# Kernel optimization log

Measured on AMD Instinct MI355X. Metric: run time of the kernel, lower is better.

## Reference

```python
import jax, jax.numpy as jnp
import numpy as np

B, IN, HID, OUT = 1024, 512, 128, 64
INP1 = IN + 1  # 513, after prepending ones column


def setup_inputs() -> dict:
    key = jax.random.key(0)
    k1, k2, k3, k4, k5, k6, k7, k8 = jax.random.split(key, 8)
    s1 = 1.0 / np.sqrt(INP1 * INP1)
    s2 = 1.0 / np.sqrt(HID)
    return {
        "img": jax.random.normal(k1, (B, IN), dtype=jnp.float32),
        "tab": jax.random.normal(k2, (B, IN), dtype=jnp.float32),
        "W1": jax.random.uniform(k3, (HID, INP1 * INP1), jnp.float32, -s1, s1),
        "b1": jax.random.uniform(k4, (HID,), jnp.float32, -s1, s1),
        "W2": jax.random.uniform(k5, (HID, HID), jnp.float32, -s2, s2),
        "b2": jax.random.uniform(k6, (HID,), jnp.float32, -s2, s2),
        "W3": jax.random.uniform(k7, (OUT, HID), jnp.float32, -s2, s2),
        "b3": jax.random.uniform(k8, (OUT,), jnp.float32, -s2, s2),
    }


def reference(img, tab, W1, b1, W2, b2, W3, b3):
    ones = jnp.ones((img.shape[0], 1), dtype=img.dtype)
    x = jnp.concatenate([ones, img], axis=1)  # [B, IN+1]
    t = jnp.concatenate([ones, tab], axis=1)  # [B, IN+1]
    # batched outer product, flattened: [B, (IN+1)*(IN+1)]
    fusion = jnp.einsum("bi,bj->bij", x, t).reshape(x.shape[0], -1)
    # dropout is identity in eval mode
    y1 = fusion @ W1.T + b1
    y2 = jnp.tanh(y1 @ W2.T + b2)
    y3 = jax.nn.relu(y2 @ W3.T + b3)
    return y3
```

## Files before the change

### kernel.cpp

```cpp
#include <hip/hip_runtime.h>
#include <hip/hip_bf16.h>

typedef __bf16 bf16x8 __attribute__((ext_vector_type(8)));
typedef float f32x4 __attribute__((ext_vector_type(4)));
typedef float f32x4u __attribute__((ext_vector_type(4), aligned(4)));
typedef unsigned short u16x8 __attribute__((ext_vector_type(8)));

typedef __attribute__((address_space(1))) const unsigned int gu32;
typedef __attribute__((address_space(3))) unsigned int lu32;

#define B_SZ   1024
#define IN_SZ  512
#define HID    128
#define OUT_SZ 64
#define BK     32
#define NKT    16

static __device__ __forceinline__ unsigned short f2bf(float f) {
    __hip_bfloat16 h = __float2bfloat16(f);
    return *reinterpret_cast<unsigned short*>(&h);
}

__global__ __launch_bounds__(256) void prep_kernel(
    const float* __restrict__ img, const float* __restrict__ tab,
    unsigned short* __restrict__ tbt, float* __restrict__ xhT,
    float* __restrict__ tc)
{
    const int blk = blockIdx.x;
    for (int j = threadIdx.x; j < 512; j += 256) {
        float v = (j == 0) ? 1.0f : tab[(size_t)blk * IN_SZ + (j - 1)];
        tbt[(size_t)blk * 512 + j] = f2bf(v);
    }
    if (threadIdx.x == 0) tc[blk] = tab[(size_t)blk * IN_SZ + 511];
    if (blk < 513) {
        for (int b = threadIdx.x; b < B_SZ; b += 256)
            xhT[(size_t)blk * B_SZ + b] =
                (blk == 0) ? 1.0f : img[(size_t)b * IN_SZ + (blk - 1)];
    }
}

__global__ __launch_bounds__(256) void prep2_kernel(
    const float* __restrict__ w1, unsigned short* __restrict__ w1b)
{
    const long long gid = (long long)blockIdx.x * 256 + threadIdx.x;
    const int r  = (int)(gid >> 6);
    const int c8 = ((int)gid & 63) << 3;
    const float* src = w1 + (size_t)r * 513 + c8;
    const f32x4u lo = *reinterpret_cast<const f32x4u*>(src);
    const f32x4u hi = *reinterpret_cast<const f32x4u*>(src + 4);
    u16x8 u;
    u[0] = f2bf(lo[0]); u[1] = f2bf(lo[1]); u[2] = f2bf(lo[2]); u[3] = f2bf(lo[3]);
    u[4] = f2bf(hi[0]); u[5] = f2bf(hi[1]); u[6] = f2bf(hi[2]); u[7] = f2bf(hi[3]);
    *reinterpret_cast<u16x8*>(w1b + (size_t)r * 512 + c8) = u;
}

__global__ __launch_bounds__(512, 4) void gemm_fused(
    const float* __restrict__ w1, const unsigned short* __restrict__ w1b,
    const unsigned short* __restrict__ tbt,
    const float* __restrict__ xhT, const float* __restrict__ tc,
    float* __restrict__ y1acc)
{
    __shared__ unsigned short Als[3][128 * BK];
    __shared__ unsigned short Bls[3][256 * BK];

    int wgid;
    {
        const int orig = blockIdx.x;
        const int xcd = orig & 7;
        const int pos = orig >> 3;
        wgid = (xcd < 4 ? xcd * 257 : 4 * 257 + (xcd - 4) * 256) + pos;
    }
    const int bm = wgid >> 2;
    const int bn = wgid & 3;
    const int m0 = bm * 128;
    const int n0 = bn * 256;
    const int tid  = threadIdx.x;
    const int wv   = tid >> 6;
    const int wr   = wv >> 2;
    const int wc   = wv & 3;
    const int lane = tid & 63;
    const int l15  = lane & 15;
    const int kg   = lane >> 4;

    const unsigned short* asrc;
    {
        const int r  = tid >> 2;
        const int cl = (tid & 3) ^ ((r >> 1) & 3);
        asrc = w1b + (size_t)(m0 + r) * 512 + cl * 8;
    }
    const int aBase = (wv * 64) * 8;

    const unsigned short* bsrc[2];
    int bBase[2];
    #pragma unroll
    for (int q = 0; q < 2; ++q) {
        const int p  = q * 512 + tid;
        const int r  = p >> 2;
        const int cl = (p & 3) ^ ((r >> 1) & 3);
        bsrc[q] = tbt + (size_t)(n0 + r) * 512 + cl * 8;
        bBase[q] = (q * 512 + wv * 64) * 8;
    }

    int aoffs[4], boffs[4];
    #pragma unroll
    for (int ms = 0; ms < 4; ++ms) {
        const int r = wr * 64 + ms * 16 + l15;
        aoffs[ms] = (r * 4 + (kg ^ ((r >> 1) & 3))) * 8;
    }
    #pragma unroll
    for (int ns = 0; ns < 4; ++ns) {
        const int r = wc * 64 + ns * 16 + l15;
        boffs[ns] = (r * 4 + (kg ^ ((r >> 1) & 3))) * 8;
    }

    f32x4 acc[4][4] = {};

#define STAGE(BUF, KT) do {                                                  \
        const int k32_ = (KT) * BK;                                          \
        __builtin_amdgcn_global_load_lds(                                    \
            (gu32*)(const void*)(asrc + k32_),                               \
            (lu32*)(void*)&Als[BUF][aBase], 16, 0, 0);                       \
        _Pragma("unroll")                                                    \
        for (int q_ = 0; q_ < 2; ++q_)                                       \
            __builtin_amdgcn_global_load_lds(                                \
                (gu32*)(const void*)(bsrc[q_] + k32_),                       \
                (lu32*)(void*)&Bls[BUF][bBase[q_]], 16, 0, 0);               \
    } while (0)

    STAGE(0, 0);
    STAGE(1, 1);

    #pragma unroll
    for (int kt = 0; kt < NKT; ++kt) {
        if (kt == NKT - 1) asm volatile("s_waitcnt vmcnt(0)" ::: "memory");
        else               asm volatile("s_waitcnt vmcnt(3)" ::: "memory");
        __builtin_amdgcn_s_barrier();
        __builtin_amdgcn_sched_barrier(0);

        if (kt + 2 < NKT) STAGE((kt + 2) % 3, kt + 2);

        const int cur = kt % 3;
        const unsigned short* ab = &Als[cur][0];
        const unsigned short* bb = &Bls[cur][0];
        bf16x8 af[4], bfr[4];
        #pragma unroll
        for (int ms = 0; ms < 4; ++ms)
            af[ms] = *reinterpret_cast<const bf16x8*>(&ab[aoffs[ms]]);
        #pragma unroll
        for (int ns = 0; ns < 4; ++ns)
            bfr[ns] = *reinterpret_cast<const bf16x8*>(&bb[boffs[ns]]);
        __builtin_amdgcn_s_setprio(1);
        #pragma unroll
        for (int ms = 0; ms < 4; ++ms)
            #pragma unroll
            for (int ns = 0; ns < 4; ++ns)
                acc[ms][ns] = __builtin_amdgcn_mfma_f32_16x16x32_bf16(
                    af[ms], bfr[ns], acc[ms][ns], 0, 0, 0);
        __builtin_amdgcn_s_setprio(0);
    }
#undef STAGE

    const int h0 = m0 / 513;
    const int mb = (h0 + 1) * 513;
    const bool cross = (mb < m0 + 128);

    float wcv[4][4];
    #pragma unroll
    for (int ms = 0; ms < 4; ++ms)
        #pragma unroll
        for (int v = 0; v < 4; ++v)
            wcv[ms][v] = w1[(size_t)(m0 + wr * 64 + ms * 16 + kg * 4 + v) * 513 + 512];

    #pragma unroll
    for (int ns = 0; ns < 4; ++ns) {
        const int ncol = n0 + wc * 64 + ns * 16 + l15;
        const float tv = tc[ncol];
        float s0 = 0.f, s1 = 0.f;
        #pragma unroll
        for (int ms = 0; ms < 4; ++ms) {
            #pragma unroll
            for (int v = 0; v < 4; ++v) {
                const int m = m0 + wr * 64 + ms * 16 + kg * 4 + v;
                const bool lo = (m < mb);
                const int i = lo ? (m - h0 * 513) : (m - mb);
                const float xv = xhT[(size_t)i * B_SZ + ncol];
                const float val = (acc[ms][ns][v] + wcv[ms][v] * tv) * xv;
                if (lo) s0 += val; else s1 += val;
            }
        }
        s0 += __shfl_xor(s0, 16); s0 += __shfl_xor(s0, 32);
        if (lane < 16) atomicAdd(&y1acc[(size_t)ncol * HID + h0], s0);
        if (cross) {
            s1 += __shfl_xor(s1, 16); s1 += __shfl_xor(s1, 32);
            if (lane < 16 && (h0 + 1) < HID)
                atomicAdd(&y1acc[(size_t)ncol * HID + h0 + 1], s1);
        }
    }
}

__global__ __launch_bounds__(512, 4) void gemm_fused_fb(
    const float* __restrict__ w1, const unsigned short* __restrict__ tbt,
    const float* __restrict__ xhT, const float* __restrict__ tc,
    float* __restrict__ y1acc)
{
    __shared__ float          Afs[2][64 * BK];
    __shared__ unsigned short Bls[2][512 * BK];

    const int bm = blockIdx.x >> 1;
    const int bn = blockIdx.x & 1;
    const int m0 = bm * 64;
    const int n0 = bn * 512;
    const int tid  = threadIdx.x;
    const int wv   = tid >> 6;
    const int lane = tid & 63;
    const int l15  = lane & 15;
    const int kg   = lane >> 4;

    const int ar  = tid >> 3;
    const int acl = (tid & 7) ^ (ar & 7);
    const float* asrc = w1 + (size_t)(m0 + ar) * 513 + acl * 4;
    const int aBase = (wv * 64) * 4;

    const unsigned short* bsrc[4];
    int bBase[4];
    #pragma unroll
    for (int q = 0; q < 4; ++q) {
        const int p  = q * 512 + tid;
        const int r  = p >> 2;
        const int cl = (p & 3) ^ ((r >> 1) & 3);
        bsrc[q] = tbt + (size_t)(n0 + r) * 512 + cl * 8;
        bBase[q] = (q * 512 + wv * 64) * 8;
    }

    int aoff0[4], aoff1[4], boffs[4];
    #pragma unroll
    for (int ms = 0; ms < 4; ++ms) {
        const int r = ms * 16 + l15;
        aoff0[ms] = r * 32 + (((kg * 2) + 0) ^ (r & 7)) * 4;
        aoff1[ms] = r * 32 + (((kg * 2) + 1) ^ (r & 7)) * 4;
    }
    #pragma unroll
    for (int ns = 0; ns < 4; ++ns) {
        const int r = wv * 64 + ns * 16 + l15;
        boffs[ns] = ((r << 2) | (kg ^ ((r >> 1) & 3))) * 8;
    }

    f32x4 acc[4][4] = {};

#define STAGE_FB(BUF, KT) do {                                               \
        const int k32_ = (KT) * BK;                                          \
        _Pragma("unroll")                                                    \
        for (int q_ = 0; q_ < 4; ++q_)                                       \
            __builtin_amdgcn_global_load_lds(                                \
                (gu32*)(const void*)(bsrc[q_] + k32_),                       \
                (lu32*)(void*)&Bls[BUF][bBase[q_]], 16, 0, 0);               \
        __builtin_amdgcn_global_load_lds(                                    \
            (gu32*)(const void*)(asrc + k32_),                               \
            (lu32*)(void*)&Afs[BUF][aBase], 16, 0, 0);                       \
    } while (0)

    STAGE_FB(0, 0);
    __syncthreads();

    for (int kt = 0; kt < NKT; ++kt) {
        const int cur = kt & 1;
        if (kt + 1 < NKT) STAGE_FB(cur ^ 1, kt + 1);

        const float*          ab = &Afs[cur][0];
        const unsigned short* bb = &Bls[cur][0];
        bf16x8 bfr[4];
        #pragma unroll
        for (int ns = 0; ns < 4; ++ns)
            bfr[ns] = *reinterpret_cast<const bf16x8*>(&bb[boffs[ns]]);
        #pragma unroll
        for (int ms = 0; ms < 4; ++ms) {
            const f32x4 lo = *reinterpret_cast<const f32x4*>(&ab[aoff0[ms]]);
            const f32x4 hi = *reinterpret_cast<const f32x4*>(&ab[aoff1[ms]]);
            u16x8 u;
            u[0] = f2bf(lo[0]); u[1] = f2bf(lo[1]);
            u[2] = f2bf(lo[2]); u[3] = f2bf(lo[3]);
            u[4] = f2bf(hi[0]); u[5] = f2bf(hi[1]);
            u[6] = f2bf(hi[2]); u[7] = f2bf(hi[3]);
            const bf16x8 af = __builtin_bit_cast(bf16x8, u);
            #pragma unroll
            for (int ns = 0; ns < 4; ++ns)
                acc[ms][ns] = __builtin_amdgcn_mfma_f32_16x16x32_bf16(
                    af, bfr[ns], acc[ms][ns], 0, 0, 0);
        }
        __syncthreads();
    }
#undef STAGE_FB

    const int h0 = m0 / 513;
    const int mb = (h0 + 1) * 513;
    const bool cross = (mb < m0 + 64);

    float wcv[4][4];
    #pragma unroll
    for (int ms = 0; ms < 4; ++ms)
        #pragma unroll
        for (int v = 0; v < 4; ++v)
            wcv[ms][v] = w1[(size_t)(m0 + ms * 16 + kg * 4 + v) * 513 + 512];

    #pragma unroll
    for (int ns = 0; ns < 4; ++ns) {
        const int ncol = n0 + wv * 64 + ns * 16 + l15;
        const float tv = tc[ncol];
        float s0 = 0.f, s1 = 0.f;
        #pragma unroll
        for (int ms = 0; ms < 4; ++ms) {
            #pragma unroll
            for (int v = 0; v < 4; ++v) {
                const int m = m0 + ms * 16 + kg * 4 + v;
                const bool lo = (m < mb);
                const int i = lo ? (m - h0 * 513) : (m - mb);
                const float xv = xhT[(size_t)i * B_SZ + ncol];
                const float val = (acc[ms][ns][v] + wcv[ms][v] * tv) * xv;
                if (lo) s0 += val; else s1 += val;
            }
        }
        s0 += __shfl_xor(s0, 16); s0 += __shfl_xor(s0, 32);
        if (lane < 16) atomicAdd(&y1acc[(size_t)ncol * HID + h0], s0);
        if (cross) {
            s1 += __shfl_xor(s1, 16); s1 += __shfl_xor(s1, 32);
            if (lane < 16 && (h0 + 1) < HID)
                atomicAdd(&y1acc[(size_t)ncol * HID + h0 + 1], s1);
        }
    }
}

__global__ __launch_bounds__(128) void mlp_kernel(
    const float* __restrict__ y1acc, const float* __restrict__ b1,
    const float* __restrict__ W2, const float* __restrict__ b2,
    const float* __restrict__ W3, const float* __restrict__ b3,
    float* __restrict__ out)
{
    __shared__ float y1r[HID];
    __shared__ float y2r[HID];
    const int b = blockIdx.x;
    const int h = threadIdx.x;
    y1r[h] = y1acc[(size_t)b * HID + h] + b1[h];
    __syncthreads();
    float a = b2[h];
    const float* w2r = W2 + (size_t)h * HID;
    #pragma unroll 8
    for (int k = 0; k < HID; ++k) a += w2r[k] * y1r[k];
    y2r[h] = tanhf(a);
    __syncthreads();
    if (h < OUT_SZ) {
        float a3 = b3[h];
        const float* w3r = W3 + (size_t)h * HID;
        #pragma unroll 8
        for (int k = 0; k < HID; ++k) a3 += w3r[k] * y2r[k];
        out[(size_t)b * OUT_SZ + h] = fmaxf(a3, 0.f);
    }
}

extern "C" void kernel_launch(void* const* d_in, const int* in_sizes, int n_in,
                              void* d_out, int out_size, void* d_ws, size_t ws_size,
                              hipStream_t stream) {
    const float* img = (const float*)d_in[0];
    const float* tab = (const float*)d_in[1];
    const float* W1  = (const float*)d_in[2];
    const float* b1  = (const float*)d_in[3];
    const float* W2  = (const float*)d_in[4];
    const float* b2  = (const float*)d_in[5];
    const float* W3  = (const float*)d_in[6];
    const float* b3  = (const float*)d_in[7];
    float* out = (float*)d_out;

    char* ws = (char*)d_ws;
    float*          y1acc = (float*)ws;
    unsigned short* tbt   = (unsigned short*)(ws + 524288);
    float*          xhT   = (float*)(ws + 1572864);
    float*          tc    = (float*)(ws + 3674112);
    unsigned short* w1b   = (unsigned short*)(ws + 3678208);
    const size_t need = 3678208ULL + 67239936ULL;

    hipMemsetAsync(y1acc, 0, (size_t)B_SZ * HID * sizeof(float), stream);
    prep_kernel<<<dim3(1024), dim3(256), 0, stream>>>(img, tab, tbt, xhT, tc);
    if (ws_size >= need) {
        prep2_kernel<<<dim3(65664 * 64 / 256), dim3(256), 0, stream>>>(W1, w1b);
        gemm_fused<<<dim3(2052), dim3(512), 0, stream>>>(W1, w1b, tbt, xhT, tc, y1acc);
    } else {
        gemm_fused_fb<<<dim3(2052), dim3(512), 0, stream>>>(W1, tbt, xhT, tc, y1acc);
    }
    mlp_kernel<<<dim3(1024), dim3(128), 0, stream>>>(y1acc, b1, W2, b2, W3, b3, out);
}
```

Before: 188.3 us.

## Enlarge W1 GEMM tile to 256x256 with BK=64 quarter-phased pipeline

The main bf16 GEMM tile grows from 128x256 to 256x256, so each workgroup holds 8x4 accumulator fragments and loads tiles with BK=64 into two double-buffered halves. A new 32-phase loop interleaves quarter-tile LDS fragment reads and global-to-LDS prefetches with MFMA blocks, aiming to raise arithmetic intensity and overlap loads with compute. W1 rows are padded to a multiple of 256 with zeros in the conversion kernel, and the grid is halved. The larger tile increases register and LDS use and cuts occupancy to 2 waves per SIMD, and it adds more barriers per k-step.

```diff
diff --git a/kernel.cpp b/kernel.cpp
--- a/kernel.cpp
+++ b/kernel.cpp
@@ -15,6 +15,8 @@
 #define OUT_SZ 64
 #define BK     32
 #define NKT    16
+#define M_REAL 65664
+#define M_PAD  65792
 
 static __device__ __forceinline__ unsigned short f2bf(float f) {
     __hip_bfloat16 h = __float2bfloat16(f);
@@ -45,34 +47,38 @@
     const long long gid = (long long)blockIdx.x * 256 + threadIdx.x;
     const int r  = (int)(gid >> 6);
     const int c8 = ((int)gid & 63) << 3;
-    const float* src = w1 + (size_t)r * 513 + c8;
-    const f32x4u lo = *reinterpret_cast<const f32x4u*>(src);
-    const f32x4u hi = *reinterpret_cast<const f32x4u*>(src + 4);
     u16x8 u;
-    u[0] = f2bf(lo[0]); u[1] = f2bf(lo[1]); u[2] = f2bf(lo[2]); u[3] = f2bf(lo[3]);
-    u[4] = f2bf(hi[0]); u[5] = f2bf(hi[1]); u[6] = f2bf(hi[2]); u[7] = f2bf(hi[3]);
+    if (r < M_REAL) {
+        const float* src = w1 + (size_t)r * 513 + c8;
+        const f32x4u lo = *reinterpret_cast<const f32x4u*>(src);
+        const f32x4u hi = *reinterpret_cast<const f32x4u*>(src + 4);
+        u[0] = f2bf(lo[0]); u[1] = f2bf(lo[1]); u[2] = f2bf(lo[2]); u[3] = f2bf(lo[3]);
+        u[4] = f2bf(hi[0]); u[5] = f2bf(hi[1]); u[6] = f2bf(hi[2]); u[7] = f2bf(hi[3]);
+    } else {
+        u = (u16x8){0,0,0,0,0,0,0,0};
+    }
     *reinterpret_cast<u16x8*>(w1b + (size_t)r * 512 + c8) = u;
 }
 
-__global__ __launch_bounds__(512, 4) void gemm_fused(
+__global__ __launch_bounds__(512, 2) void gemm_fused(
     const float* __restrict__ w1, const unsigned short* __restrict__ w1b,
     const unsigned short* __restrict__ tbt,
     const float* __restrict__ xhT, const float* __restrict__ tc,
     float* __restrict__ y1acc)
 {
-    __shared__ unsigned short Als[3][128 * BK];
-    __shared__ unsigned short Bls[3][256 * BK];
+    __shared__ unsigned short Als[2 * 2 * 8192];
+    __shared__ unsigned short Bls[2 * 2 * 8192];
 
     int wgid;
     {
         const int orig = blockIdx.x;
         const int xcd = orig & 7;
         const int pos = orig >> 3;
-        wgid = (xcd < 4 ? xcd * 257 : 4 * 257 + (xcd - 4) * 256) + pos;
+        wgid = (xcd < 4 ? xcd * 129 : 4 * 129 + (xcd - 4) * 128) + pos;
     }
     const int bm = wgid >> 2;
     const int bn = wgid & 3;
-    const int m0 = bm * 128;
+    const int m0 = bm * 256;
     const int n0 = bn * 256;
     const int tid  = threadIdx.x;
     const int wv   = tid >> 6;
@@ -82,109 +88,153 @@
     const int l15  = lane & 15;
     const int kg   = lane >> 4;
 
-    const unsigned short* asrc;
-    {
-        const int r  = tid >> 2;
-        const int cl = (tid & 3) ^ ((r >> 1) & 3);
-        asrc = w1b + (size_t)(m0 + r) * 512 + cl * 8;
-    }
-    const int aBase = (wv * 64) * 8;
-
-    const unsigned short* bsrc[2];
-    int bBase[2];
-    #pragma unroll
-    for (int q = 0; q < 2; ++q) {
-        const int p  = q * 512 + tid;
-        const int r  = p >> 2;
-        const int cl = (p & 3) ^ ((r >> 1) & 3);
-        bsrc[q] = tbt + (size_t)(n0 + r) * 512 + cl * 8;
-        bBase[q] = (q * 512 + wv * 64) * 8;
-    }
-
-    int aoffs[4], boffs[4];
-    #pragma unroll
-    for (int ms = 0; ms < 4; ++ms) {
-        const int r = wr * 64 + ms * 16 + l15;
-        aoffs[ms] = (r * 4 + (kg ^ ((r >> 1) & 3))) * 8;
-    }
-    #pragma unroll
-    for (int ns = 0; ns < 4; ++ns) {
-        const int r = wc * 64 + ns * 16 + l15;
-        boffs[ns] = (r * 4 + (kg ^ ((r >> 1) & 3))) * 8;
-    }
-
-    f32x4 acc[4][4] = {};
-
-#define STAGE(BUF, KT) do {                                                  \
-        const int k32_ = (KT) * BK;                                          \
-        __builtin_amdgcn_global_load_lds(                                    \
-            (gu32*)(const void*)(asrc + k32_),                               \
-            (lu32*)(void*)&Als[BUF][aBase], 16, 0, 0);                       \
-        _Pragma("unroll")                                                    \
-        for (int q_ = 0; q_ < 2; ++q_)                                       \
-            __builtin_amdgcn_global_load_lds(                                \
-                (gu32*)(const void*)(bsrc[q_] + k32_),                       \
-                (lu32*)(void*)&Bls[BUF][bBase[q_]], 16, 0, 0);               \
+    const unsigned short* aS[2][2];
+    int aD[2];
+    const unsigned short* bS[2][2];
+    int bD[2];
+    #pragma unroll
+    for (int cq = 0; cq < 2; ++cq) {
+        const int p  = cq * 512 + tid;
+        const int rr = p >> 3;
+        const int lc = (p & 7) ^ (rr & 7);
+        {
+            const int wr_ = rr >> 6, j = rr & 63;
+            aS[cq][0] = w1b + (size_t)(m0 + wr_ * 128 +      j) * 512 + lc * 8;
+            aS[cq][1] = w1b + (size_t)(m0 + wr_ * 128 + 64 + j) * 512 + lc * 8;
+        }
+        {
+            const int wc_ = rr >> 5, j2 = rr & 31;
+            bS[cq][0] = tbt + (size_t)(n0 + wc_ * 64 +      j2) * 512 + lc * 8;
+            bS[cq][1] = tbt + (size_t)(n0 + wc_ * 64 + 32 + j2) * 512 + lc * 8;
+        }
+        aD[cq] = p * 8;
+        bD[cq] = p * 8;
+    }
+
+    int aoff[4][2], boff[2][2];
+    #pragma unroll
+    for (int mf = 0; mf < 4; ++mf)
+        #pragma unroll
+        for (int ks = 0; ks < 2; ++ks) {
+            const int rr = wr * 64 + mf * 16 + l15;
+            aoff[mf][ks] = rr * 64 + ((ks * 4 + kg) ^ (rr & 7)) * 8;
+        }
+    #pragma unroll
+    for (int fr = 0; fr < 2; ++fr)
+        #pragma unroll
+        for (int ks = 0; ks < 2; ++ks) {
+            const int rr = wc * 32 + fr * 16 + l15;
+            boff[fr][ks] = rr * 64 + ((ks * 4 + kg) ^ (rr & 7)) * 8;
+        }
+
+    f32x4 acc[8][4] = {};
+    bf16x8 fA[4][2], fB[2][2][2];
+
+#define GL(SRC, DST) __builtin_amdgcn_global_load_lds(                       \
+        (gu32*)(const void*)(SRC), (lu32*)(void*)(DST), 16, 0, 0)
+#define STA(T, H) do {                                                       \
+        unsigned short* b_ = &Als[((((T) & 1) << 1) + (H)) * 8192];          \
+        GL(aS[0][H] + (T) * 64, b_ + aD[0]);                                 \
+        GL(aS[1][H] + (T) * 64, b_ + aD[1]);                                 \
     } while (0)
-
-    STAGE(0, 0);
-    STAGE(1, 1);
-
-    #pragma unroll
-    for (int kt = 0; kt < NKT; ++kt) {
-        if (kt == NKT - 1) asm volatile("s_waitcnt vmcnt(0)" ::: "memory");
-        else               asm volatile("s_waitcnt vmcnt(3)" ::: "memory");
+#define STB(T, H) do {                                                       \
+        unsigned short* b_ = &Bls[((((T) & 1) << 1) + (H)) * 8192];          \
+        GL(bS[0][H] + (T) * 64, b_ + bD[0]);                                 \
+        GL(bS[1][H] + (T) * 64, b_ + bD[1]);                                 \
+    } while (0)
+
+    STA(0, 0); STB(0, 0); STA(0, 1); STB(0, 1); STA(1, 0); STB(1, 0);
+    asm volatile("s_waitcnt vmcnt(4)" ::: "memory");
+    __builtin_amdgcn_s_barrier();
+
+    #pragma unroll
+    for (int P = 0; P < 32; ++P) {
+        const int kt = P >> 2, q = P & 3, d = kt & 1, mh = q >> 1, nq = q & 1;
+        const unsigned short* Ab = &Als[((d << 1) + mh) * 8192];
+        const unsigned short* Bb = &Bls[((d << 1) + nq) * 8192];
+
+        if (q == 0) {
+            #pragma unroll
+            for (int mf = 0; mf < 4; ++mf)
+                #pragma unroll
+                for (int ks = 0; ks < 2; ++ks)
+                    fA[mf][ks] = *reinterpret_cast<const bf16x8*>(&Ab[aoff[mf][ks]]);
+            #pragma unroll
+            for (int fr = 0; fr < 2; ++fr)
+                #pragma unroll
+                for (int ks = 0; ks < 2; ++ks)
+                    fB[0][fr][ks] = *reinterpret_cast<const bf16x8*>(&Bb[boff[fr][ks]]);
+            if (kt + 1 <= 7) STA(kt + 1, 1);
+        } else if (q == 1) {
+            #pragma unroll
+            for (int fr = 0; fr < 2; ++fr)
+                #pragma unroll
+                for (int ks = 0; ks < 2; ++ks)
+                    fB[1][fr][ks] = *reinterpret_cast<const bf16x8*>(&Bb[boff[fr][ks]]);
+            if (kt + 1 <= 7) STB(kt + 1, 1);
+        } else if (q == 2) {
+            #pragma unroll
+            for (int mf = 0; mf < 4; ++mf)
+                #pragma unroll
+                for (int ks = 0; ks < 2; ++ks)
+                    fA[mf][ks] = *reinterpret_cast<const bf16x8*>(&Ab[aoff[mf][ks]]);
+            if (kt + 2 <= 7) STA(kt + 2, 0);
+        } else {
+            if (kt + 2 <= 7) STB(kt + 2, 0);
+        }
+
         __builtin_amdgcn_s_barrier();
+        asm volatile("s_waitcnt lgkmcnt(0)" ::: "memory");
         __builtin_amdgcn_sched_barrier(0);
-
-        if (kt + 2 < NKT) STAGE((kt + 2) % 3, kt + 2);
-
-        const int cur = kt % 3;
-        const unsigned short* ab = &Als[cur][0];
-        const unsigned short* bb = &Bls[cur][0];
-        bf16x8 af[4], bfr[4];
-        #pragma unroll
-        for (int ms = 0; ms < 4; ++ms)
-            af[ms] = *reinterpret_cast<const bf16x8*>(&ab[aoffs[ms]]);
-        #pragma unroll
-        for (int ns = 0; ns < 4; ++ns)
-            bfr[ns] = *reinterpret_cast<const bf16x8*>(&bb[boffs[ns]]);
         __builtin_amdgcn_s_setprio(1);
         #pragma unroll
-        for (int ms = 0; ms < 4; ++ms)
-            #pragma unroll
-            for (int ns = 0; ns < 4; ++ns)
-                acc[ms][ns] = __builtin_amdgcn_mfma_f32_16x16x32_bf16(
-                    af[ms], bfr[ns], acc[ms][ns], 0, 0, 0);
+        for (int mf = 0; mf < 4; ++mf)
+            #pragma unroll
+            for (int fr = 0; fr < 2; ++fr)
+                #pragma unroll
+                for (int ks = 0; ks < 2; ++ks)
+                    acc[mh * 4 + mf][nq * 2 + fr] =
+                        __builtin_amdgcn_mfma_f32_16x16x32_bf16(
+                            fA[mf][ks], fB[nq][fr][ks],
+                            acc[mh * 4 + mf][nq * 2 + fr], 0, 0, 0);
         __builtin_amdgcn_s_setprio(0);
-    }
-#undef STAGE
+        if (q == 3) {
+            if (kt >= 6) asm volatile("s_waitcnt vmcnt(0)" ::: "memory");
+            else         asm volatile("s_waitcnt vmcnt(4)" ::: "memory");
+        }
+        __builtin_amdgcn_s_barrier();
+    }
+#undef STA
+#undef STB
+#undef GL
 
     const int h0 = m0 / 513;
     const int mb = (h0 + 1) * 513;
-    const bool cross = (mb < m0 + 128);
-
-    float wcv[4][4];
-    #pragma unroll
-    for (int ms = 0; ms < 4; ++ms)
-        #pragma unroll
-        for (int v = 0; v < 4; ++v)
-            wcv[ms][v] = w1[(size_t)(m0 + wr * 64 + ms * 16 + kg * 4 + v) * 513 + 512];
-
-    #pragma unroll
-    for (int ns = 0; ns < 4; ++ns) {
-        const int ncol = n0 + wc * 64 + ns * 16 + l15;
+    const bool cross = (mb < m0 + 256);
+
+    float wcv[8][4];
+    #pragma unroll
+    for (int am = 0; am < 8; ++am)
+        #pragma unroll
+        for (int v = 0; v < 4; ++v) {
+            const int g = m0 + wr * 128 + am * 16 + kg * 4 + v;
+            wcv[am][v] = (g < M_REAL) ? w1[(size_t)g * 513 + 512] : 0.f;
+        }
+
+    #pragma unroll
+    for (int an = 0; an < 4; ++an) {
+        const int ncol = n0 + wc * 64 + an * 16 + l15;
         const float tv = tc[ncol];
         float s0 = 0.f, s1 = 0.f;
         #pragma unroll
-        for (int ms = 0; ms < 4; ++ms) {
+        for (int am = 0; am < 8; ++am) {
             #pragma unroll
             for (int v = 0; v < 4; ++v) {
-                const int m = m0 + wr * 64 + ms * 16 + kg * 4 + v;
+                const int m = m0 + wr * 128 + am * 16 + kg * 4 + v;
                 const bool lo = (m < mb);
                 const int i = lo ? (m - h0 * 513) : (m - mb);
-                const float xv = xhT[(size_t)i * B_SZ + ncol];
-                const float val = (acc[ms][ns][v] + wcv[ms][v] * tv) * xv;
+                const float val = (acc[am][an][v] + wcv[am][v] * tv)
+                                  * xhT[(size_t)i * B_SZ + ncol];
                 if (lo) s0 += val; else s1 += val;
             }
         }
@@ -314,8 +364,8 @@
                 const int m = m0 + ms * 16 + kg * 4 + v;
                 const bool lo = (m < mb);
                 const int i = lo ? (m - h0 * 513) : (m - mb);
-                const float xv = xhT[(size_t)i * B_SZ + ncol];
-                const float val = (acc[ms][ns][v] + wcv[ms][v] * tv) * xv;
+                const float val = (acc[ms][ns][v] + wcv[ms][v] * tv)
+                                  * xhT[(size_t)i * B_SZ + ncol];
                 if (lo) s0 += val; else s1 += val;
             }
         }
@@ -375,13 +425,13 @@
     float*          xhT   = (float*)(ws + 1572864);
     float*          tc    = (float*)(ws + 3674112);
     unsigned short* w1b   = (unsigned short*)(ws + 3678208);
-    const size_t need = 3678208ULL + 67239936ULL;
+    const size_t need = 3678208ULL + 67371008ULL;
 
     hipMemsetAsync(y1acc, 0, (size_t)B_SZ * HID * sizeof(float), stream);
     prep_kernel<<<dim3(1024), dim3(256), 0, stream>>>(img, tab, tbt, xhT, tc);
     if (ws_size >= need) {
-        prep2_kernel<<<dim3(65664 * 64 / 256), dim3(256), 0, stream>>>(W1, w1b);
-        gemm_fused<<<dim3(2052), dim3(512), 0, stream>>>(W1, w1b, tbt, xhT, tc, y1acc);
+        prep2_kernel<<<dim3(M_PAD * 64 / 256), dim3(256), 0, stream>>>(W1, w1b);
+        gemm_fused<<<dim3(1028), dim3(512), 0, stream>>>(W1, w1b, tbt, xhT, tc, y1acc);
     } else {
         gemm_fused_fb<<<dim3(2052), dim3(512), 0, stream>>>(W1, tbt, xhT, tc, y1acc);
     }
```

Measured after the change: 222.1 us. 1.18x slower.

## Split W1 rows into aligned 512-row GEMM blocks plus separate tail kernel

Applied to the files above, without the earlier changes.

Reorganizes the W1 bf16 copy so that each hidden unit contributes exactly 512 rows (i=0..511), which makes every 128-row GEMM tile map to a single hidden unit. The straddle logic (two partial sums and a second atomic) and the irregular XCD remap are removed, and the grid drops to 2048 blocks. The leftover i=512 row of each hidden unit is handled by a new small tail kernel that uses a transposed copy of those weights. The cost is two extra kernel launches (prep3 and tail) and more atomics into y1acc.

```diff
diff --git a/kernel.cpp b/kernel.cpp
--- a/kernel.cpp
+++ b/kernel.cpp
@@ -15,6 +15,7 @@
 #define OUT_SZ 64
 #define BK     32
 #define NKT    16
+#define M2     65536
 
 static __device__ __forceinline__ unsigned short f2bf(float f) {
     __hip_bfloat16 h = __float2bfloat16(f);
@@ -40,22 +41,33 @@
 }
 
 __global__ __launch_bounds__(256) void prep2_kernel(
-    const float* __restrict__ w1, unsigned short* __restrict__ w1b)
+    const float* __restrict__ w1, unsigned short* __restrict__ w1c)
 {
     const long long gid = (long long)blockIdx.x * 256 + threadIdx.x;
     const int r  = (int)(gid >> 6);
     const int c8 = ((int)gid & 63) << 3;
-    const float* src = w1 + (size_t)r * 513 + c8;
+    const size_t srow = (size_t)(r >> 9) * 513 + (r & 511);
+    const float* src = w1 + srow * 513 + c8;
     const f32x4u lo = *reinterpret_cast<const f32x4u*>(src);
     const f32x4u hi = *reinterpret_cast<const f32x4u*>(src + 4);
     u16x8 u;
     u[0] = f2bf(lo[0]); u[1] = f2bf(lo[1]); u[2] = f2bf(lo[2]); u[3] = f2bf(lo[3]);
     u[4] = f2bf(hi[0]); u[5] = f2bf(hi[1]); u[6] = f2bf(hi[2]); u[7] = f2bf(hi[3]);
-    *reinterpret_cast<u16x8*>(w1b + (size_t)r * 512 + c8) = u;
+    *reinterpret_cast<u16x8*>(w1c + (size_t)r * 512 + c8) = u;
+}
+
+__global__ __launch_bounds__(256) void prep3_kernel(
+    const float* __restrict__ w1, float* __restrict__ wrowT)
+{
+    const int idx = blockIdx.x * 256 + threadIdx.x;
+    if (idx < 513 * 128) {
+        const int j = idx >> 7, h = idx & 127;
+        wrowT[idx] = w1[((size_t)h * 513 + 512) * 513 + j];
+    }
 }
 
 __global__ __launch_bounds__(512, 4) void gemm_fused(
-    const float* __restrict__ w1, const unsigned short* __restrict__ w1b,
+    const float* __restrict__ w1, const unsigned short* __restrict__ w1c,
     const unsigned short* __restrict__ tbt,
     const float* __restrict__ xhT, const float* __restrict__ tc,
     float* __restrict__ y1acc)
@@ -63,13 +75,7 @@
     __shared__ unsigned short Als[3][128 * BK];
     __shared__ unsigned short Bls[3][256 * BK];
 
-    int wgid;
-    {
-        const int orig = blockIdx.x;
-        const int xcd = orig & 7;
-        const int pos = orig >> 3;
-        wgid = (xcd < 4 ? xcd * 257 : 4 * 257 + (xcd - 4) * 256) + pos;
-    }
+    const int wgid = (blockIdx.x & 7) * 256 + (blockIdx.x >> 3);
     const int bm = wgid >> 2;
     const int bn = wgid & 3;
     const int m0 = bm * 128;
@@ -86,7 +92,7 @@
     {
         const int r  = tid >> 2;
         const int cl = (tid & 3) ^ ((r >> 1) & 3);
-        asrc = w1b + (size_t)(m0 + r) * 512 + cl * 8;
+        asrc = w1c + (size_t)(m0 + r) * 512 + cl * 8;
     }
     const int aBase = (wv * 64) * 8;
 
@@ -160,42 +166,60 @@
     }
 #undef STAGE
 
-    const int h0 = m0 / 513;
-    const int mb = (h0 + 1) * 513;
-    const bool cross = (mb < m0 + 128);
+    const int h0    = bm >> 2;
+    const int ibase = (bm & 3) * 128;
+    const size_t orow = (size_t)h0 * 513;
 
     float wcv[4][4];
     #pragma unroll
     for (int ms = 0; ms < 4; ++ms)
         #pragma unroll
-        for (int v = 0; v < 4; ++v)
-            wcv[ms][v] = w1[(size_t)(m0 + wr * 64 + ms * 16 + kg * 4 + v) * 513 + 512];
+        for (int v = 0; v < 4; ++v) {
+            const int i_ = ibase + wr * 64 + ms * 16 + kg * 4 + v;
+            wcv[ms][v] = w1[(orow + i_) * 513 + 512];
+        }
 
     #pragma unroll
     for (int ns = 0; ns < 4; ++ns) {
         const int ncol = n0 + wc * 64 + ns * 16 + l15;
         const float tv = tc[ncol];
-        float s0 = 0.f, s1 = 0.f;
+        float s0 = 0.f;
         #pragma unroll
         for (int ms = 0; ms < 4; ++ms) {
+            const int i_ = ibase + wr * 64 + ms * 16 + kg * 4;
             #pragma unroll
-            for (int v = 0; v < 4; ++v) {
-                const int m = m0 + wr * 64 + ms * 16 + kg * 4 + v;
-                const bool lo = (m < mb);
-                const int i = lo ? (m - h0 * 513) : (m - mb);
-                const float xv = xhT[(size_t)i * B_SZ + ncol];
-                const float val = (acc[ms][ns][v] + wcv[ms][v] * tv) * xv;
-                if (lo) s0 += val; else s1 += val;
-            }
+            for (int v = 0; v < 4; ++v)
+                s0 += (acc[ms][ns][v] + wcv[ms][v] * tv)
+                      * xhT[(size_t)(i_ + v) * B_SZ + ncol];
         }
         s0 += __shfl_xor(s0, 16); s0 += __shfl_xor(s0, 32);
         if (lane < 16) atomicAdd(&y1acc[(size_t)ncol * HID + h0], s0);
-        if (cross) {
-            s1 += __shfl_xor(s1, 16); s1 += __shfl_xor(s1, 32);
-            if (lane < 16 && (h0 + 1) < HID)
-                atomicAdd(&y1acc[(size_t)ncol * HID + h0 + 1], s1);
-        }
-    }
+    }
+}
+
+__global__ __launch_bounds__(128) void tail_kernel(
+    const float* __restrict__ img, const float* __restrict__ tab,
+    const float* __restrict__ wrowT, float* __restrict__ y1acc)
+{
+    __shared__ float tls[4][513];
+    const int b0 = blockIdx.x * 4;
+    const int h  = threadIdx.x;
+    #pragma unroll
+    for (int q = 0; q < 4; ++q)
+        for (int j = h; j < 513; j += 128)
+            tls[q][j] = (j == 0) ? 1.0f : tab[(size_t)(b0 + q) * IN_SZ + (j - 1)];
+    __syncthreads();
+    float a0 = 0.f, a1 = 0.f, a2 = 0.f, a3 = 0.f;
+    #pragma unroll 8
+    for (int j = 0; j < 513; ++j) {
+        const float w = wrowT[j * 128 + h];
+        a0 += w * tls[0][j]; a1 += w * tls[1][j];
+        a2 += w * tls[2][j]; a3 += w * tls[3][j];
+    }
+    atomicAdd(&y1acc[(size_t)(b0 + 0) * HID + h], a0 * img[(size_t)(b0 + 0) * IN_SZ + 511]);
+    atomicAdd(&y1acc[(size_t)(b0 + 1) * HID + h], a1 * img[(size_t)(b0 + 1) * IN_SZ + 511]);
+    atomicAdd(&y1acc[(size_t)(b0 + 2) * HID + h], a2 * img[(size_t)(b0 + 2) * IN_SZ + 511]);
+    atomicAdd(&y1acc[(size_t)(b0 + 3) * HID + h], a3 * img[(size_t)(b0 + 3) * IN_SZ + 511]);
 }
 
 __global__ __launch_bounds__(512, 4) void gemm_fused_fb(
@@ -314,8 +338,8 @@
                 const int m = m0 + ms * 16 + kg * 4 + v;
                 const bool lo = (m < mb);
                 const int i = lo ? (m - h0 * 513) : (m - mb);
-                const float xv = xhT[(size_t)i * B_SZ + ncol];
-                const float val = (acc[ms][ns][v] + wcv[ms][v] * tv) * xv;
+                const float val = (acc[ms][ns][v] + wcv[ms][v] * tv)
+                                  * xhT[(size_t)i * B_SZ + ncol];
                 if (lo) s0 += val; else s1 += val;
             }
         }
@@ -374,14 +398,17 @@
     unsigned short* tbt   = (unsigned short*)(ws + 524288);
     float*          xhT   = (float*)(ws + 1572864);
     float*          tc    = (float*)(ws + 3674112);
-    unsigned short* w1b   = (unsigned short*)(ws + 3678208);
-    const size_t need = 3678208ULL + 67239936ULL;
+    float*          wrowT = (float*)(ws + 3678208);
+    unsigned short* w1c   = (unsigned short*)(ws + 3940864);
+    const size_t need = 3940864ULL + 67108864ULL;
 
     hipMemsetAsync(y1acc, 0, (size_t)B_SZ * HID * sizeof(float), stream);
     prep_kernel<<<dim3(1024), dim3(256), 0, stream>>>(img, tab, tbt, xhT, tc);
     if (ws_size >= need) {
-        prep2_kernel<<<dim3(65664 * 64 / 256), dim3(256), 0, stream>>>(W1, w1b);
-        gemm_fused<<<dim3(2052), dim3(512), 0, stream>>>(W1, w1b, tbt, xhT, tc, y1acc);
+        prep2_kernel<<<dim3(M2 * 64 / 256), dim3(256), 0, stream>>>(W1, w1c);
+        prep3_kernel<<<dim3(257), dim3(256), 0, stream>>>(W1, wrowT);
+        gemm_fused<<<dim3(2048), dim3(512), 0, stream>>>(W1, w1c, tbt, xhT, tc, y1acc);
+        tail_kernel<<<dim3(256), dim3(128), 0, stream>>>(img, tab, wrowT, y1acc);
     } else {
         gemm_fused_fb<<<dim3(2052), dim3(512), 0, stream>>>(W1, tbt, xhT, tc, y1acc);
     }
```

After: 216.2 us. 1.15x slower.
